# Kernel optimization log

Measured on AMD Instinct MI355X. Metric: run time of the kernel, lower is better.

## Reference

```python
import jax, jax.numpy as jnp
import numpy as np

HEAD_DIM = 64
HIDDEN_SIZE = 2880
NUM_HEADS = 64
NUM_KV_HEADS = 8
INPUT_SIZE = 2 * HIDDEN_SIZE


def _rotate_half(x):
    x1, x2 = jnp.split(x, 2, axis=-1)
    return jnp.concatenate([-x2, x1], axis=-1)


def _apply_rotary_emb(x, cos, sin):
    return x * cos + _rotate_half(x) * sin


def setup_inputs() -> dict:
    key = jax.random.key(0)
    ks = jax.random.split(key, 7)
    B, S = 1, 2048
    hidden_states = jax.random.normal(ks[0], (B, S, INPUT_SIZE), dtype=jnp.float32)
    cos = jax.random.uniform(ks[1], (1, 1, S, HEAD_DIM), dtype=jnp.float32)
    sin = jax.random.uniform(ks[2], (1, 1, S, HEAD_DIM), dtype=jnp.float32)
    sc = 1.0 / np.sqrt(INPUT_SIZE)
    wq = jax.random.normal(ks[3], (INPUT_SIZE, NUM_HEADS * HEAD_DIM), dtype=jnp.float32) * sc
    wk = jax.random.normal(ks[4], (INPUT_SIZE, NUM_KV_HEADS * HEAD_DIM), dtype=jnp.float32) * sc
    wv = jax.random.normal(ks[5], (INPUT_SIZE, NUM_KV_HEADS * HEAD_DIM), dtype=jnp.float32) * sc
    wo = jax.random.normal(ks[6], (NUM_HEADS * HEAD_DIM, HIDDEN_SIZE), dtype=jnp.float32) * (1.0 / np.sqrt(NUM_HEADS * HEAD_DIM))
    return {"hidden_states": hidden_states, "cos": cos, "sin": sin,
            "wq": wq, "wk": wk, "wv": wv, "wo": wo}


def reference(hidden_states, cos, sin, wq, wk, wv, wo):
    B, S, _ = hidden_states.shape
    # projections -> [B, H, S, D]
    q = (hidden_states @ wq).reshape(B, S, NUM_HEADS, HEAD_DIM).transpose(0, 2, 1, 3)
    k = (hidden_states @ wk).reshape(B, S, NUM_KV_HEADS, HEAD_DIM).transpose(0, 2, 1, 3)
    v = (hidden_states @ wv).reshape(B, S, NUM_KV_HEADS, HEAD_DIM).transpose(0, 2, 1, 3)
    q = _apply_rotary_emb(q, cos, sin)
    k = _apply_rotary_emb(k, cos, sin)
    # GQA expand KV heads: [B, Hkv, S, D] -> [B, H, S, D]
    groups = NUM_HEADS // NUM_KV_HEADS
    k = jnp.repeat(k, groups, axis=1)
    v = jnp.repeat(v, groups, axis=1)
    scale = 1.0 / np.sqrt(HEAD_DIM).astype(np.float32)
    attn = jnp.einsum('bhqd,bhkd->bhqk', q, k) * scale  # [B,H,S,S]
    attn = jax.nn.softmax(attn.astype(jnp.float32), axis=-1).astype(q.dtype)
    out = jnp.einsum('bhqk,bhkd->bhqd', attn, v)
    out = out.transpose(0, 2, 1, 3).reshape(B, S, NUM_HEADS * HEAD_DIM)
    return out @ wo
```

## Files before the change

### kernel.cpp

```cpp
#include <hip/hip_runtime.h>
#include <hip/hip_bf16.h>

#define SEQ   2048
#define INSZ  5760
#define NQ    4096
#define NKV   512
#define NQKV  5120
#define HQ    64
#define HKV   8
#define HD    64
#define HID   2880
#define HIDP  2944

typedef __attribute__((ext_vector_type(8))) short bf16x8;
typedef __attribute__((ext_vector_type(4))) float f32x4;
typedef __attribute__((ext_vector_type(16))) float f32x16;
typedef unsigned int u32;

__device__ __forceinline__ unsigned short f2bf(float x) {
  __hip_bfloat16 b = __float2bfloat16(x);
  return __builtin_bit_cast(unsigned short, b);
}
__device__ __forceinline__ float bf2f(unsigned short u) {
  return __bfloat162float(__builtin_bit_cast(__hip_bfloat16, u));
}
__device__ __forceinline__ float exp2_hw(float x) {
  float r;
  asm("v_exp_f32 %0, %1" : "=v"(r) : "v"(x));
  return r;
}
__device__ __forceinline__ u32 cvt_pk_bf16(float lo, float hi) {
  u32 r;
  asm("v_cvt_pk_bf16_f32 %0, %1, %2" : "=v"(r) : "v"(lo), "v"(hi));
  return r;
}

__global__ void k_convert(const float* __restrict__ src, unsigned short* __restrict__ dst, int n) {
  int stride = gridDim.x * blockDim.x * 4;
  for (int idx = (blockIdx.x * blockDim.x + threadIdx.x) * 4; idx < n; idx += stride) {
    float4 v = *(const float4*)(src + idx);
    ushort4 o;
    o.x = f2bf(v.x); o.y = f2bf(v.y); o.z = f2bf(v.z); o.w = f2bf(v.w);
    *(ushort4*)(dst + idx) = o;
  }
}

__global__ void k_tconv(const float* __restrict__ src, unsigned short* __restrict__ dst,
                        int K, int N) {
  __shared__ float tile[64][33];
  int k0 = blockIdx.x * 64, n0 = blockIdx.y * 32;
  int tid = threadIdx.x;
  int r = tid >> 5, c = tid & 31;
#pragma unroll
  for (int i = 0; i < 8; i++) {
    int row = i * 8 + r;
    tile[row][c] = (n0 + c < N) ? src[(size_t)(k0 + row) * N + n0 + c] : 0.f;
  }
  __syncthreads();
  int n = tid >> 3, kk = (tid & 7) * 8;
  union { u32 w[4]; bf16x8 v; } u;
#pragma unroll
  for (int j = 0; j < 4; j++)
    u.w[j] = cvt_pk_bf16(tile[kk + 2 * j][n], tile[kk + 2 * j + 1][n]);
  *(bf16x8*)(dst + (size_t)(n0 + n) * K + k0 + kk) = u.v;
}

template <typename OutT>
__global__ __launch_bounds__(256) void k_gemm_bt(
    const unsigned short* __restrict__ A,
    const unsigned short* __restrict__ BT,
    OutT* __restrict__ C, int Kdim, int Ncols, int ldc) {
  __shared__ unsigned short sA[2][128 * 32];
  __shared__ unsigned short sB[2][128 * 32];
  int tid = threadIdx.x, wid = tid >> 6, lane = tid & 63;
  int gx = gridDim.x;
  int nwg = gx * gridDim.y;
  int lin = blockIdx.y * gx + blockIdx.x;
  int qn = nwg >> 3, rn = nwg & 7;
  int xcd = lin & 7, idx = lin >> 3;
  int swz = (xcd < rn ? xcd * (qn + 1) : rn * (qn + 1) + (xcd - rn) * qn) + idx;
  int bm = swz % gx, bn = swz / gx;
  const unsigned short* Ab = A + (size_t)bm * 128 * Kdim;
  const unsigned short* Bb = BT + (size_t)bn * 128 * Kdim;
  f32x4 acc[4][4];
#pragma unroll
  for (int i = 0; i < 4; i++)
#pragma unroll
    for (int j = 0; j < 4; j++) acc[i][j] = f32x4{0.f, 0.f, 0.f, 0.f};
  int wr = (wid >> 1) * 64, wc = (wid & 1) * 64;
  int srow = lane >> 2;
  int selem = (lane & 3) * 8;
  int rbase = lane & 15, koff = (lane >> 4) * 8;

#define G_STAGE(buf, kt)                                                             \
  {                                                                                  \
    _Pragma("unroll") for (int ch2 = 0; ch2 < 2; ++ch2) {                            \
      int chunk = wid * 2 + ch2;                                                     \
      const unsigned short* ga = Ab + (size_t)(chunk * 16 + srow) * Kdim + (kt) + selem; \
      const unsigned short* gb = Bb + (size_t)(chunk * 16 + srow) * Kdim + (kt) + selem; \
      __builtin_amdgcn_global_load_lds(                                              \
          (const __attribute__((address_space(1))) void*)ga,                         \
          (__attribute__((address_space(3))) void*)(&sA[buf][chunk * 512]), 16, 0, 0); \
      __builtin_amdgcn_global_load_lds(                                              \
          (const __attribute__((address_space(1))) void*)gb,                         \
          (__attribute__((address_space(3))) void*)(&sB[buf][chunk * 512]), 16, 0, 0); \
    }                                                                                \
  }

  int nt = Kdim >> 5;
  G_STAGE(0, 0);
  __syncthreads();
  int cur = 0;
  for (int t = 0; t < nt; ++t) {
    if (t + 1 < nt) G_STAGE(cur ^ 1, (t + 1) * 32);
    bf16x8 a[4], b[4];
#pragma unroll
    for (int i = 0; i < 4; i++)
      a[i] = *(const bf16x8*)(&sA[cur][(wr + i * 16 + rbase) * 32 + koff]);
#pragma unroll
    for (int j = 0; j < 4; j++)
      b[j] = *(const bf16x8*)(&sB[cur][(wc + j * 16 + rbase) * 32 + koff]);
#pragma unroll
    for (int i = 0; i < 4; i++)
#pragma unroll
      for (int j = 0; j < 4; j++)
        acc[i][j] = __builtin_amdgcn_mfma_f32_16x16x32_bf16(a[i], b[j], acc[i][j], 0, 0, 0);
    __syncthreads();
    cur ^= 1;
  }
#undef G_STAGE
  int rw = (lane >> 4) * 4, cl = lane & 15;
#pragma unroll
  for (int i = 0; i < 4; i++)
#pragma unroll
    for (int j = 0; j < 4; j++) {
      int col = bn * 128 + wc + j * 16 + cl;
      if (col < Ncols) {
#pragma unroll
        for (int r = 0; r < 4; r++) {
          int row = bm * 128 + wr + i * 16 + rw + r;
          float v = acc[i][j][r];
          if constexpr (sizeof(OutT) == 2)
            C[(size_t)row * ldc + col] = (OutT)f2bf(v);
          else
            C[(size_t)row * ldc + col] = v;
        }
      }
    }
}

__global__ void k_rope(unsigned short* __restrict__ qkv, const float* __restrict__ cosb,
                       const float* __restrict__ sinb) {
  int s = blockIdx.x;
  const float* cs = cosb + s * HD;
  const float* sn = sinb + s * HD;
  unsigned short* row = qkv + (size_t)s * NQKV;
  for (int idx = threadIdx.x; idx < (HQ + HKV) * 32; idx += blockDim.x) {
    int head = idx >> 5, dp = idx & 31;
    unsigned short* base = row + (head < HQ ? head * 64 : NQ + (head - HQ) * 64);
    float x1 = bf2f(base[dp]), x2 = bf2f(base[dp + 32]);
    float o1 = x1 * cs[dp] - x2 * sn[dp];
    float o2 = x2 * cs[dp + 32] + x1 * sn[dp + 32];
    base[dp] = f2bf(o1);
    base[dp + 32] = f2bf(o2);
  }
}

__global__ void k_vtrans(const unsigned short* __restrict__ qkv, unsigned short* __restrict__ vt) {
  __shared__ unsigned short tile[64 * 66];
  int st = blockIdx.x, hk = blockIdx.y;
  int s0 = st * 64, t = threadIdx.x;
#pragma unroll
  for (int i = 0; i < 16; i++) {
    int e = i * 256 + t;
    int sl = e >> 6, d = e & 63;
    tile[d * 66 + sl] = qkv[(size_t)(s0 + sl) * NQKV + NQ + NKV + hk * 64 + d];
  }
  __syncthreads();
#pragma unroll
  for (int i = 0; i < 16; i++) {
    int e = i * 256 + t;
    int d = e >> 6, sl = e & 63;
    vt[(size_t)(hk * 64 + d) * SEQ + s0 + sl] = tile[d * 66 + sl];
  }
}

__global__ __launch_bounds__(256) void k_attn(
    const unsigned short* __restrict__ qkv, const unsigned short* __restrict__ vt,
    unsigned short* __restrict__ out) {
  __shared__ unsigned short smem[16384];
  int tid = threadIdx.x, wid = tid >> 6, lane = tid & 63;
  int head = blockIdx.x, qt = blockIdx.y;
  int hkv = head >> 3;
  int q = lane & 31, h = lane >> 5;
  int q0w = qt * 128 + wid * 32;
  const float SL2 = 0.125f * 1.44269504f;

  bf16x8 qf[4];
  {
    const unsigned short* qrow = qkv + (size_t)(q0w + q) * NQKV + head * 64 + h * 8;
#pragma unroll
    for (int ks = 0; ks < 4; ks++) qf[ks] = *(const bf16x8*)(qrow + ks * 16);
  }

  int r8 = lane >> 3;
  int srcslot = ((lane & 7) ^ r8) * 16;
  int sw = q & 7;

#define STAGE_KV(buf, kv)                                                            \
  {                                                                                  \
    _Pragma("unroll") for (int ch = 0; ch < 2; ++ch) {                               \
      int r0 = (wid * 2 + ch) * 8;                                                   \
      const char* gk =                                                               \
          (const char*)(qkv + (size_t)((kv) + r0 + r8) * NQKV + NQ + hkv * 64) +     \
          srcslot;                                                                   \
      __builtin_amdgcn_global_load_lds(                                              \
          (const __attribute__((address_space(1))) void*)gk,                         \
          (__attribute__((address_space(3))) void*)(smem + (buf)*4096 + r0 * 64),    \
          16, 0, 0);                                                                 \
      const char* gv =                                                               \
          (const char*)(vt + (size_t)(hkv * 64 + r0 + r8) * SEQ + (kv)) + srcslot;   \
      __builtin_amdgcn_global_load_lds(                                              \
          (const __attribute__((address_space(1))) void*)gv,                         \
          (__attribute__((address_space(3))) void*)(smem + 8192 + (buf)*4096 +       \
                                                    r0 * 64),                        \
          16, 0, 0);                                                                 \
    }                                                                                \
  }

  f32x16 o0, o1;
#pragma unroll
  for (int r = 0; r < 16; r++) { o0[r] = 0.f; o1[r] = 0.f; }
  float m = -3e38f, lp = 0.f;

  STAGE_KV(0, 0);
  __syncthreads();
  int cur = 0;

  for (int kvt = 0; kvt < SEQ / 64; ++kvt) {
    if (kvt + 1 < SEQ / 64) STAGE_KV(cur ^ 1, (kvt + 1) * 64);
    const char* kb = (const char*)(smem + cur * 4096);
    const char* vb = (const char*)(smem + 8192 + cur * 4096);

    f32x16 st0, st1;
#pragma unroll
    for (int r = 0; r < 16; r++) { st0[r] = 0.f; st1[r] = 0.f; }
    {
      bf16x8 kf[4];
#pragma unroll
      for (int ks = 0; ks < 4; ks++)
        kf[ks] = *(const bf16x8*)(kb + q * 128 + (((2 * ks + h) ^ sw) << 4));
#pragma unroll
      for (int ks = 0; ks < 4; ks++)
        st0 = __builtin_amdgcn_mfma_f32_32x32x16_bf16(kf[ks], qf[ks], st0, 0, 0, 0);
#pragma unroll
      for (int ks = 0; ks < 4; ks++)
        kf[ks] = *(const bf16x8*)(kb + (32 + q) * 128 + (((2 * ks + h) ^ sw) << 4));
#pragma unroll
      for (int ks = 0; ks < 4; ks++)
        st1 = __builtin_amdgcn_mfma_f32_32x32x16_bf16(kf[ks], qf[ks], st1, 0, 0, 0);
    }

    float tmx[16];
#pragma unroll
    for (int r = 0; r < 16; r++) tmx[r] = fmaxf(st0[r], st1[r]);
#pragma unroll
    for (int s = 8; s >= 1; s >>= 1)
#pragma unroll
      for (int r = 0; r < 8; r++)
        if (r < s) tmx[r] = fmaxf(tmx[r], tmx[r + s]);
    float mx = fmaxf(tmx[0], __shfl_xor(tmx[0], 32, 64));
    float t2 = mx * SL2;

    if (__any(t2 > m + 8.f)) {
      float mn = fmaxf(m, t2);
      float corr = exp2_hw(m - mn);
      m = mn;
      lp *= corr;
#pragma unroll
      for (int r = 0; r < 16; r++) { o0[r] *= corr; o1[r] *= corr; }
    }

    float psa[4] = {0.f, 0.f, 0.f, 0.f};
#pragma unroll
    for (int r = 0; r < 16; r++) {
      float e0 = exp2_hw(fmaf(st0[r], SL2, -m));
      float e1 = exp2_hw(fmaf(st1[r], SL2, -m));
      st0[r] = e0; st1[r] = e1;
      psa[r & 3] += e0 + e1;
    }
    lp += (psa[0] + psa[1]) + (psa[2] + psa[3]);

    u32 pk[16];
#pragma unroll
    for (int w = 0; w < 8; w++) {
      pk[w] = cvt_pk_bf16(st0[2 * w], st0[2 * w + 1]);
      pk[8 + w] = cvt_pk_bf16(st1[2 * w], st1[2 * w + 1]);
    }

    bf16x8 pf[4];
#pragma unroll
    for (int ks = 0; ks < 4; ks++) {
      int base = 8 * (ks >> 1) + 4 * (ks & 1);
      u32 wA0 = pk[base], wA1 = pk[base + 1], wB0 = pk[base + 2], wB1 = pk[base + 3];
      u32 keep0 = h ? wB0 : wA0, keep1 = h ? wB1 : wA1;
      u32 send0 = h ? wA0 : wB0, send1 = h ? wA1 : wB1;
      u32 rc0 = (u32)__shfl_xor((int)send0, 32, 64);
      u32 rc1 = (u32)__shfl_xor((int)send1, 32, 64);
      union { u32 w[4]; bf16x8 v; } u;
      u.w[0] = h ? rc0 : keep0;
      u.w[1] = h ? rc1 : keep1;
      u.w[2] = h ? keep0 : rc0;
      u.w[3] = h ? keep1 : rc1;
      pf[ks] = u.v;
    }

    {
      bf16x8 vf[4];
#pragma unroll
      for (int ks = 0; ks < 4; ks++)
        vf[ks] = *(const bf16x8*)(vb + q * 128 + (((2 * ks + h) ^ sw) << 4));
#pragma unroll
      for (int ks = 0; ks < 4; ks++)
        o0 = __builtin_amdgcn_mfma_f32_32x32x16_bf16(vf[ks], pf[ks], o0, 0, 0, 0);
#pragma unroll
      for (int ks = 0; ks < 4; ks++)
        vf[ks] = *(const bf16x8*)(vb + (32 + q) * 128 + (((2 * ks + h) ^ sw) << 4));
#pragma unroll
      for (int ks = 0; ks < 4; ks++)
        o1 = __builtin_amdgcn_mfma_f32_32x32x16_bf16(vf[ks], pf[ks], o1, 0, 0, 0);
    }

    __syncthreads();
    cur ^= 1;
  }

  float lpt = lp + __shfl_xor(lp, 32, 64);
  float inv = 1.0f / lpt;

  unsigned short* ot = smem + wid * (32 * 72);
#pragma unroll
  for (int w = 0; w < 8; w++) {
    int reg = 2 * w;
    int dbase = (reg & 3) + 8 * (reg >> 2) + 4 * h;
    u32 p0 = cvt_pk_bf16(o0[reg] * inv, o0[reg + 1] * inv);
    u32 p1 = cvt_pk_bf16(o1[reg] * inv, o1[reg + 1] * inv);
    *(u32*)(ot + q * 72 + dbase) = p0;
    *(u32*)(ot + q * 72 + 32 + dbase) = p1;
  }
  __syncthreads();
  int row = lane >> 1, halfc = lane & 1;
  const unsigned short* src = ot + row * 72 + halfc * 32;
  unsigned short* dst = out + (size_t)(q0w + row) * NQ + head * 64 + halfc * 32;
#pragma unroll
  for (int c = 0; c < 4; c++)
    *(bf16x8*)(dst + c * 8) = *(const bf16x8*)(src + c * 8);
#undef STAGE_KV
}

extern "C" void kernel_launch(void* const* d_in, const int* in_sizes, int n_in,
                              void* d_out, int out_size, void* d_ws, size_t ws_size,
                              hipStream_t stream) {
  const float* hidden = (const float*)d_in[0];
  const float* cosb = (const float*)d_in[1];
  const float* sinb = (const float*)d_in[2];
  const float* wq = (const float*)d_in[3];
  const float* wk = (const float*)d_in[4];
  const float* wv = (const float*)d_in[5];
  const float* wo = (const float*)d_in[6];
  float* out = (float*)d_out;

  unsigned short* hb = (unsigned short*)d_ws;
  unsigned short* qkv = hb + (size_t)SEQ * INSZ;
  unsigned short* wqkvT = qkv + (size_t)SEQ * NQKV;
  unsigned short* woT = wqkvT + (size_t)NQKV * INSZ;
  unsigned short* vt = woT + (size_t)HIDP * NQ;
  unsigned short* attn = vt + (size_t)NKV * SEQ;

  k_convert<<<dim3(1024), dim3(256), 0, stream>>>(hidden, hb, SEQ * INSZ);
  k_tconv<<<dim3(INSZ / 64, NQ / 32), dim3(256), 0, stream>>>(wq, wqkvT, INSZ, NQ);
  k_tconv<<<dim3(INSZ / 64, NKV / 32), dim3(256), 0, stream>>>(
      wk, wqkvT + (size_t)NQ * INSZ, INSZ, NKV);
  k_tconv<<<dim3(INSZ / 64, NKV / 32), dim3(256), 0, stream>>>(
      wv, wqkvT + (size_t)(NQ + NKV) * INSZ, INSZ, NKV);
  k_tconv<<<dim3(NQ / 64, HIDP / 32), dim3(256), 0, stream>>>(wo, woT, NQ, HID);

  k_gemm_bt<unsigned short><<<dim3(SEQ / 128, NQKV / 128), dim3(256), 0, stream>>>(
      hb, wqkvT, qkv, INSZ, NQKV, NQKV);
  k_rope<<<dim3(SEQ), dim3(256), 0, stream>>>(qkv, cosb, sinb);
  k_vtrans<<<dim3(SEQ / 64, HKV), dim3(256), 0, stream>>>(qkv, vt);
  k_attn<<<dim3(HQ, SEQ / 128), dim3(256), 0, stream>>>(qkv, vt, attn);
  k_gemm_bt<float><<<dim3(SEQ / 128, (HID + 127) / 128), dim3(256), 0, stream>>>(
      attn, woT, out, NQ, HID, HID);
}
```

Baseline: 624.7 us.

## Add 256x256-tile QKV GEMM with direct global-to-LDS loads and swizzled LDS

Replaces the 128x128-tile QKV projection GEMM with a new kernel. It uses 256x256 output tiles, 512 threads and a double-buffered pipeline. Tiles are loaded straight from global memory into LDS with global_load_lds, and the LDS layout is XOR-swizzled. Wave priority is raised around the MFMA blocks. The goal is more data reuse per block and less load-instruction and register traffic. The trade-off is that the grid shrinks to 160 workgroups, which can leave many compute units idle on a large GPU.

```diff
diff --git a/kernel.cpp b/kernel.cpp
--- a/kernel.cpp
+++ b/kernel.cpp
@@ -63,6 +63,119 @@
   for (int j = 0; j < 4; j++)
     u.w[j] = cvt_pk_bf16(tile[kk + 2 * j][n], tile[kk + 2 * j + 1][n]);
   *(bf16x8*)(dst + (size_t)(n0 + n) * K + k0 + kk) = u.v;
+}
+
+__global__ __launch_bounds__(512, 2) void k_gemm8(
+    const unsigned short* __restrict__ A,
+    const unsigned short* __restrict__ BT,
+    unsigned short* __restrict__ C, int Kd, int ldc) {
+  __shared__ __align__(16) char smem[65536];
+  int tid = threadIdx.x, wid = tid >> 6, lane = tid & 63;
+  int wr = wid >> 2, wc = wid & 3;
+  int nwg = gridDim.x * gridDim.y;
+  int lin = blockIdx.y * gridDim.x + blockIdx.x;
+  int qn = nwg >> 3;
+  int swz = (lin & 7) * qn + (lin >> 3);
+  int bm = swz % gridDim.x, bn = swz / gridDim.x;
+  const char* Ab = (const char*)(A + (size_t)bm * 256 * Kd);
+  const char* Bb = (const char*)(BT + (size_t)bn * 256 * Kd);
+  size_t Kb = (size_t)Kd * 2;
+
+  int L0 = wid * 1024 + lane * 16;
+  int L1 = L0 + 8192;
+  int sr0 = L0 >> 6, sr1 = L1 >> 6;
+  int si0 = (L0 & 63) ^ ((sr0 & 3) << 4);
+  int si1 = (L1 & 63) ^ ((sr1 & 3) << 4);
+  const char* gA0 = Ab + (size_t)sr0 * Kb + si0;
+  const char* gA1 = Ab + (size_t)sr1 * Kb + si1;
+  const char* gB0 = Bb + (size_t)sr0 * Kb + si0;
+  const char* gB1 = Bb + (size_t)sr1 * Kb + si1;
+
+#define STAGE8(t, buf)                                                               \
+  {                                                                                  \
+    int kb = (t) * 64;                                                               \
+    char* dA = smem + (buf) * 32768;                                                 \
+    char* dB = dA + 16384;                                                           \
+    __builtin_amdgcn_global_load_lds(                                                \
+        (const __attribute__((address_space(1))) void*)(gA0 + kb),                   \
+        (__attribute__((address_space(3))) void*)(dA + L0), 16, 0, 0);               \
+    __builtin_amdgcn_global_load_lds(                                                \
+        (const __attribute__((address_space(1))) void*)(gA1 + kb),                   \
+        (__attribute__((address_space(3))) void*)(dA + L1), 16, 0, 0);               \
+    __builtin_amdgcn_global_load_lds(                                                \
+        (const __attribute__((address_space(1))) void*)(gB0 + kb),                   \
+        (__attribute__((address_space(3))) void*)(dB + L0), 16, 0, 0);               \
+    __builtin_amdgcn_global_load_lds(                                                \
+        (const __attribute__((address_space(1))) void*)(gB1 + kb),                   \
+        (__attribute__((address_space(3))) void*)(dB + L1), 16, 0, 0);               \
+  }
+
+  f32x4 acc[8][4];
+#pragma unroll
+  for (int i = 0; i < 8; i++)
+#pragma unroll
+    for (int j = 0; j < 4; j++) acc[i][j] = f32x4{0.f, 0.f, 0.f, 0.f};
+
+  int rA = wr * 128 + (lane & 15);
+  int rB = wc * 64 + (lane & 15);
+  int xA = (((lane >> 4) ^ rA) & 3) << 4;
+  int xB = (((lane >> 4) ^ rB) & 3) << 4;
+
+  int nt = Kd >> 5;
+  STAGE8(0, 0);
+  for (int t = 0; t < nt; ++t) {
+    int c = t & 1;
+    if (t + 1 < nt) {
+      STAGE8(t + 1, c ^ 1);
+      asm volatile("s_waitcnt vmcnt(4)" ::: "memory");
+    } else {
+      asm volatile("s_waitcnt vmcnt(0)" ::: "memory");
+    }
+    __builtin_amdgcn_sched_barrier(0);
+    asm volatile("s_barrier" ::: "memory");
+    const char* bA = smem + c * 32768;
+    const char* bB = bA + 16384;
+    bf16x8 b[4], a[4];
+#pragma unroll
+    for (int nf = 0; nf < 4; nf++)
+      b[nf] = *(const bf16x8*)(bB + ((rB + nf * 16) << 6) + xB);
+#pragma unroll
+    for (int mf = 0; mf < 4; mf++)
+      a[mf] = *(const bf16x8*)(bA + ((rA + mf * 16) << 6) + xA);
+    __builtin_amdgcn_s_setprio(1);
+#pragma unroll
+    for (int mf = 0; mf < 4; mf++)
+#pragma unroll
+      for (int nf = 0; nf < 4; nf++)
+        acc[mf][nf] = __builtin_amdgcn_mfma_f32_16x16x32_bf16(a[mf], b[nf], acc[mf][nf], 0, 0, 0);
+    __builtin_amdgcn_s_setprio(0);
+    asm volatile("s_barrier" ::: "memory");
+#pragma unroll
+    for (int mf = 0; mf < 4; mf++)
+      a[mf] = *(const bf16x8*)(bA + ((rA + 64 + mf * 16) << 6) + xA);
+    __builtin_amdgcn_s_setprio(1);
+#pragma unroll
+    for (int mf = 0; mf < 4; mf++)
+#pragma unroll
+      for (int nf = 0; nf < 4; nf++)
+        acc[4 + mf][nf] = __builtin_amdgcn_mfma_f32_16x16x32_bf16(a[mf], b[nf], acc[4 + mf][nf], 0, 0, 0);
+    __builtin_amdgcn_s_setprio(0);
+    asm volatile("s_barrier" ::: "memory");
+  }
+#undef STAGE8
+
+  int rw = (lane >> 4) * 4, cl = lane & 15;
+#pragma unroll
+  for (int mf = 0; mf < 8; mf++)
+#pragma unroll
+    for (int nf = 0; nf < 4; nf++) {
+      int col = bn * 256 + wc * 64 + nf * 16 + cl;
+#pragma unroll
+      for (int r = 0; r < 4; r++) {
+        int row = bm * 256 + wr * 128 + mf * 16 + rw + r;
+        C[(size_t)row * ldc + col] = f2bf(acc[mf][nf][r]);
+      }
+    }
 }
 
 template <typename OutT>
@@ -385,8 +498,8 @@
       wv, wqkvT + (size_t)(NQ + NKV) * INSZ, INSZ, NKV);
   k_tconv<<<dim3(NQ / 64, HIDP / 32), dim3(256), 0, stream>>>(wo, woT, NQ, HID);
 
-  k_gemm_bt<unsigned short><<<dim3(SEQ / 128, NQKV / 128), dim3(256), 0, stream>>>(
-      hb, wqkvT, qkv, INSZ, NQKV, NQKV);
+  k_gemm8<<<dim3(SEQ / 256, NQKV / 256), dim3(512), 0, stream>>>(
+      hb, wqkvT, qkv, INSZ, NQKV);
   k_rope<<<dim3(SEQ), dim3(256), 0, stream>>>(qkv, cosb, sinb);
   k_vtrans<<<dim3(SEQ / 64, HKV), dim3(256), 0, stream>>>(qkv, vt);
   k_attn<<<dim3(HQ, SEQ / 128), dim3(256), 0, stream>>>(qkv, vt, attn);
```

New measurement: 653.7 us. +4.7%, slower.
